# Kernel tuning notes

Measured on AMD Instinct MI355X. Metric: run time of the kernel, lower is better.

The kernel has to match this reference:

```python
import jax, jax.numpy as jnp
import numpy as np

N, IN_C, OUT_C = 4096, 256, 64
ALPHA = 0.2  # LeakyReLU negative slope


def setup_inputs() -> dict:
    key = jax.random.key(0)
    k1, k2, k3, k4 = jax.random.split(key, 4)
    H = jax.random.normal(k1, (N, IN_C), dtype=jnp.float32)
    adj = jax.random.randint(k2, (N, N), 0, 2, dtype=jnp.int32)
    # xavier_uniform with gain=1.414
    gain = 1.414
    limW = gain * np.sqrt(6.0 / (IN_C + OUT_C))
    W = jax.random.uniform(k3, (IN_C, OUT_C), minval=-limW, maxval=limW, dtype=jnp.float32)
    lima = gain * np.sqrt(6.0 / (2 * OUT_C + 1))
    a = jax.random.uniform(k4, (2 * OUT_C, 1), minval=-lima, maxval=lima, dtype=jnp.float32)
    return {"H": H, "adj": adj, "W": W, "a": a}


def reference(H, adj, W, a):
    Wh = H @ W  # [N, out_C]
    # Attention_Mat[i,j] = concat(Wh_i, Wh_j); score = Attention_Mat @ a
    # = (Wh @ a1)_i + (Wh @ a2)_j  -- fused, avoids the O(N^2 * 2F) tensor.
    a1, a2 = a[:OUT_C, 0], a[OUT_C:, 0]
    e = (Wh @ a1)[:, None] + (Wh @ a2)[None, :]  # [N, N]
    e = jnp.where(e > 0, e, ALPHA * e)  # LeakyReLU
    att = jax.nn.softmax(e, axis=1)
    # NOTE: original masks AFTER softmax (rows are not renormalized).
    att = jnp.where(adj > 0, att, jnp.zeros_like(att))
    out = att @ Wh  # [N, out_C]
    return jax.nn.elu(out)  # concat=True
```

## Files before the change

kernel.cpp:

```cpp
#include <hip/hip_runtime.h>
#include <math.h>

static constexpr int NN   = 4096;
static constexpr int INC  = 256;
static constexpr int OUTC = 64;

typedef _Float16 half8 __attribute__((ext_vector_type(8)));
typedef float floatx4 __attribute__((ext_vector_type(4)));

__device__ __forceinline__ float lrelu(float x) {
    return fmaxf(x, 0.f) + 0.2f * fminf(x, 0.f);
}
__device__ __forceinline__ float elu1(float x) {
    return x > 0.f ? x : (__expf(x) - 1.f);
}

__global__ __launch_bounds__(256) void k_prep(const int* __restrict__ adj,
                                              unsigned int* __restrict__ bits,
                                              const float* __restrict__ H,
                                              const float* __restrict__ W,
                                              const float* __restrict__ a,
                                              unsigned short* __restrict__ WhT,
                                              float* __restrict__ f1,
                                              float* __restrict__ f2) {
    const int t = threadIdx.x;
    if (blockIdx.x >= 256) {
        const int tau = (blockIdx.x - 256) * 256 + t;
        const int4* src = (const int4*)adj + (size_t)tau * 8;
        unsigned int o = 0;
        #pragma unroll
        for (int u = 0; u < 8; ++u) {
            const int4 v = src[u];
            const unsigned int nib = (unsigned int)(v.x > 0)
                                   | ((unsigned int)(v.y > 0) << 1)
                                   | ((unsigned int)(v.z > 0) << 2)
                                   | ((unsigned int)(v.w > 0) << 3);
            o |= nib << (4 * u);
        }
        bits[tau] = o;
        return;
    }
    __shared__ __align__(16) float Hl[16 * INC];
    __shared__ _Float16 Tl[16 * 68];
    const int i0 = blockIdx.x * 16;
    {
        const float4* H4 = (const float4*)(H + i0 * INC);
        float4* Hl4 = (float4*)Hl;
        #pragma unroll
        for (int u = 0; u < 4; ++u) Hl4[u * 256 + t] = H4[u * 256 + t];
    }
    __syncthreads();
    const int c = t & 63;
    const int g = t >> 6;
    const float a1c = a[c];
    const float a2c = a[OUTC + c];
    float acc[4] = {0.f, 0.f, 0.f, 0.f};
    const float4* Hl4 = (const float4*)Hl;
    #pragma unroll 4
    for (int k4 = 0; k4 < INC / 4; ++k4) {
        const float w0 = W[(k4 * 4 + 0) * OUTC + c];
        const float w1 = W[(k4 * 4 + 1) * OUTC + c];
        const float w2 = W[(k4 * 4 + 2) * OUTC + c];
        const float w3 = W[(k4 * 4 + 3) * OUTC + c];
        #pragma unroll
        for (int s = 0; s < 4; ++s) {
            const float4 h = Hl4[(g + 4 * s) * (INC / 4) + k4];
            acc[s] = fmaf(h.x, w0, fmaf(h.y, w1, fmaf(h.z, w2, fmaf(h.w, w3, acc[s]))));
        }
    }
    #pragma unroll
    for (int s = 0; s < 4; ++s) {
        const int r = g + 4 * s;
        Tl[r * 68 + c] = (_Float16)acc[s];
        float v1 = acc[s] * a1c;
        float v2 = acc[s] * a2c;
        #pragma unroll
        for (int off = 32; off; off >>= 1) {
            v1 += __shfl_xor(v1, off);
            v2 += __shfl_xor(v2, off);
        }
        if (c == 0) { f1[i0 + r] = v1; f2[i0 + r] = v2; }
    }
    __syncthreads();
    const int c2 = t >> 2;
    const int rs = (t & 3) * 4;
    ushort4 u;
    u.x = *(const unsigned short*)&Tl[(rs + 0) * 68 + c2];
    u.y = *(const unsigned short*)&Tl[(rs + 1) * 68 + c2];
    u.z = *(const unsigned short*)&Tl[(rs + 2) * 68 + c2];
    u.w = *(const unsigned short*)&Tl[(rs + 3) * 68 + c2];
    *(ushort4*)(WhT + c2 * NN + i0 + rs) = u;
}

__global__ __launch_bounds__(1024, 4) void k_att(const unsigned char* __restrict__ bits,
                                                 const _Float16* __restrict__ WhT,
                                                 const float* __restrict__ f1,
                                                 const float* __restrict__ f2,
                                                 float* __restrict__ out) {
    __shared__ __align__(16) float sf2[NN];
    __shared__ __align__(16) float sacc[16 * 1024];
    __shared__ float sden[16 * 16];
    __shared__ float smax[16];
    const int t = threadIdx.x;
    const int w = t >> 6;
    const int l = t & 63;
    const int m = l & 15;
    const int quad = l >> 4;
    const int i0 = blockIdx.x * 16;

    {
        const float4 v = ((const float4*)f2)[t];
        ((float4*)sf2)[t] = v;
        float mloc = fmaxf(fmaxf(v.x, v.y), fmaxf(v.z, v.w));
        #pragma unroll
        for (int off = 32; off; off >>= 1) mloc = fmaxf(mloc, __shfl_xor(mloc, off));
        if (l == 0) smax[w] = mloc;
    }
    __syncthreads();
    float maxf2 = smax[0];
    #pragma unroll
    for (int k = 1; k < 16; ++k) maxf2 = fmaxf(maxf2, smax[k]);

    const float f1r = f1[i0 + m];
    const float mrow = lrelu(f1r + maxf2);
    float den = 0.f;
    floatx4 acc[4] = {{0.f,0.f,0.f,0.f},{0.f,0.f,0.f,0.f},{0.f,0.f,0.f,0.f},{0.f,0.f,0.f,0.f}};
    const int jbase = w * 32 + quad * 8;
    const unsigned char* brow = bits + (size_t)(i0 + m) * (NN / 8) + (jbase >> 3);
    unsigned int m8[8];
    #pragma unroll
    for (int it = 0; it < 8; ++it) m8[it] = brow[it * 64];

    #pragma unroll 2
    for (int it = 0; it < 8; ++it) {
        const int j = jbase + it * 512;
        const unsigned int mb = m8[it];
        const float4 g0 = *(const float4*)(sf2 + j);
        const float4 g1 = *(const float4*)(sf2 + j + 4);
        half8 af;
        {
            float p;
            p = __expf(lrelu(f1r + g0.x) - mrow); den += p; af[0] = (mb & 1u)   ? (_Float16)p : (_Float16)0.f;
            p = __expf(lrelu(f1r + g0.y) - mrow); den += p; af[1] = (mb & 2u)   ? (_Float16)p : (_Float16)0.f;
            p = __expf(lrelu(f1r + g0.z) - mrow); den += p; af[2] = (mb & 4u)   ? (_Float16)p : (_Float16)0.f;
            p = __expf(lrelu(f1r + g0.w) - mrow); den += p; af[3] = (mb & 8u)   ? (_Float16)p : (_Float16)0.f;
            p = __expf(lrelu(f1r + g1.x) - mrow); den += p; af[4] = (mb & 16u)  ? (_Float16)p : (_Float16)0.f;
            p = __expf(lrelu(f1r + g1.y) - mrow); den += p; af[5] = (mb & 32u)  ? (_Float16)p : (_Float16)0.f;
            p = __expf(lrelu(f1r + g1.z) - mrow); den += p; af[6] = (mb & 64u)  ? (_Float16)p : (_Float16)0.f;
            p = __expf(lrelu(f1r + g1.w) - mrow); den += p; af[7] = (mb & 128u) ? (_Float16)p : (_Float16)0.f;
        }
        #pragma unroll
        for (int nt = 0; nt < 4; ++nt) {
            const half8 bf = *(const half8*)(WhT + (size_t)(nt * 16 + m) * NN + j);
            acc[nt] = __builtin_amdgcn_mfma_f32_16x16x32_f16(af, bf, acc[nt], 0, 0, 0);
        }
    }
    den += __shfl_xor(den, 16);
    den += __shfl_xor(den, 32);
    if (l < 16) sden[w * 16 + l] = den;
    #pragma unroll
    for (int nt = 0; nt < 4; ++nt)
        #pragma unroll
        for (int r = 0; r < 4; ++r)
            sacc[w * 1024 + (quad * 4 + r) * 64 + nt * 16 + m] = acc[nt][r];
    __syncthreads();
    float s = 0.f;
    #pragma unroll
    for (int w2 = 0; w2 < 16; ++w2) s += sacc[w2 * 1024 + t];
    float dden = 0.f;
    const int row = t >> 6;
    #pragma unroll
    for (int w2 = 0; w2 < 16; ++w2) dden += sden[w2 * 16 + row];
    out[(size_t)i0 * OUTC + t] = elu1(s / dden);
}

extern "C" void kernel_launch(void* const* d_in, const int* in_sizes, int n_in,
                              void* d_out, int out_size, void* d_ws, size_t ws_size,
                              hipStream_t stream) {
    const float* H  = (const float*)d_in[0];
    const int* adj  = (const int*)d_in[1];
    const float* W  = (const float*)d_in[2];
    const float* a  = (const float*)d_in[3];
    float* out = (float*)d_out;
    char* ws = (char*)d_ws;
    unsigned short* WhT = (unsigned short*)(ws);
    float* f1 = (float*)(ws + (512 << 10));
    float* f2 = (float*)(ws + (528 << 10));
    unsigned int* bits = (unsigned int*)(ws + (1 << 20));
    hipLaunchKernelGGL(k_prep, dim3(2304), dim3(256), 0, stream,
                       adj, bits, H, W, a, WhT, f1, f2);
    hipLaunchKernelGGL(k_att,  dim3(256),  dim3(1024), 0, stream,
                       (const unsigned char*)bits, (const _Float16*)WhT, f1, f2, out);
}
```

Measured before the change: 123.5 us.

## Fuse prep and attention kernels into one cooperative kernel with grid sync

Merges the projection/mask-packing kernel and the attention kernel into a single cooperative launch separated by a grid-wide barrier. Each block now packs the adjacency bits for its own 16 rows straight into shared memory, so the packed mask no longer makes a round trip through global memory. f1 also stays in shared memory. The cost is a grid synchronization, a less coalesced per-wave adjacency read pattern, and a Wh computation that reads W from global per thread instead of staging H in shared memory.

```diff
diff --git a/kernel.cpp b/kernel.cpp
--- a/kernel.cpp
+++ b/kernel.cpp
@@ -1,5 +1,8 @@
 #include <hip/hip_runtime.h>
+#include <hip/hip_cooperative_groups.h>
 #include <math.h>
+
+namespace cg = cooperative_groups;
 
 static constexpr int NN   = 4096;
 static constexpr int INC  = 256;
@@ -15,101 +18,84 @@
     return x > 0.f ? x : (__expf(x) - 1.f);
 }
 
-__global__ __launch_bounds__(256) void k_prep(const int* __restrict__ adj,
-                                              unsigned int* __restrict__ bits,
-                                              const float* __restrict__ H,
-                                              const float* __restrict__ W,
-                                              const float* __restrict__ a,
-                                              unsigned short* __restrict__ WhT,
-                                              float* __restrict__ f1,
-                                              float* __restrict__ f2) {
+__global__ __launch_bounds__(1024, 4) void k_gat(const int* __restrict__ adj,
+                                                 const float* __restrict__ H,
+                                                 const float* __restrict__ W,
+                                                 const float* __restrict__ a,
+                                                 unsigned short* __restrict__ WhT,
+                                                 float* __restrict__ f2g,
+                                                 float* __restrict__ out) {
+    __shared__ __align__(16) float sf2[NN];
+    __shared__ __align__(16) float sacc[16 * 1024];
+    __shared__ __align__(8) unsigned long long smask[16 * 65];
+    __shared__ float sden[16 * 16];
+    __shared__ float smax[16];
+    __shared__ float sf1[16];
+
     const int t = threadIdx.x;
-    if (blockIdx.x >= 256) {
-        const int tau = (blockIdx.x - 256) * 256 + t;
-        const int4* src = (const int4*)adj + (size_t)tau * 8;
-        unsigned int o = 0;
-        #pragma unroll
-        for (int u = 0; u < 8; ++u) {
-            const int4 v = src[u];
-            const unsigned int nib = (unsigned int)(v.x > 0)
-                                   | ((unsigned int)(v.y > 0) << 1)
-                                   | ((unsigned int)(v.z > 0) << 2)
-                                   | ((unsigned int)(v.w > 0) << 3);
-            o |= nib << (4 * u);
+    const int w = t >> 6;
+    const int l = t & 63;
+    const int i0 = blockIdx.x * 16;
+    const int row = i0 + w;
+
+    {
+        const int4* ap = (const int4*)(adj + (size_t)row * NN) + l * 16;
+        unsigned long long bits = 0ull;
+        #pragma unroll 4
+        for (int k = 0; k < 16; ++k) {
+            const int4 v = ap[k];
+            const unsigned long long nib =
+                  (unsigned long long)(v.x > 0)
+                | ((unsigned long long)(v.y > 0) << 1)
+                | ((unsigned long long)(v.z > 0) << 2)
+                | ((unsigned long long)(v.w > 0) << 3);
+            bits |= nib << (4 * k);
         }
-        bits[tau] = o;
-        return;
+        smask[w * 65 + l] = bits;
     }
-    __shared__ __align__(16) float Hl[16 * INC];
-    __shared__ _Float16 Tl[16 * 68];
-    const int i0 = blockIdx.x * 16;
+
     {
-        const float4* H4 = (const float4*)(H + i0 * INC);
-        float4* Hl4 = (float4*)Hl;
-        #pragma unroll
-        for (int u = 0; u < 4; ++u) Hl4[u * 256 + t] = H4[u * 256 + t];
-    }
-    __syncthreads();
-    const int c = t & 63;
-    const int g = t >> 6;
-    const float a1c = a[c];
-    const float a2c = a[OUTC + c];
-    float acc[4] = {0.f, 0.f, 0.f, 0.f};
-    const float4* Hl4 = (const float4*)Hl;
-    #pragma unroll 4
-    for (int k4 = 0; k4 < INC / 4; ++k4) {
-        const float w0 = W[(k4 * 4 + 0) * OUTC + c];
-        const float w1 = W[(k4 * 4 + 1) * OUTC + c];
-        const float w2 = W[(k4 * 4 + 2) * OUTC + c];
-        const float w3 = W[(k4 * 4 + 3) * OUTC + c];
-        #pragma unroll
-        for (int s = 0; s < 4; ++s) {
-            const float4 h = Hl4[(g + 4 * s) * (INC / 4) + k4];
-            acc[s] = fmaf(h.x, w0, fmaf(h.y, w1, fmaf(h.z, w2, fmaf(h.w, w3, acc[s]))));
+        _Float16* Tl = (_Float16*)sacc;
+        const int c = l;
+        const float4* Hr = (const float4*)(H + (size_t)row * INC);
+        float acc = 0.f;
+        #pragma unroll 8
+        for (int k4 = 0; k4 < INC / 4; ++k4) {
+            const float4 h = Hr[k4];
+            acc = fmaf(h.x, W[(k4 * 4 + 0) * OUTC + c],
+                  fmaf(h.y, W[(k4 * 4 + 1) * OUTC + c],
+                  fmaf(h.z, W[(k4 * 4 + 2) * OUTC + c],
+                  fmaf(h.w, W[(k4 * 4 + 3) * OUTC + c], acc))));
         }
-    }
-    #pragma unroll
-    for (int s = 0; s < 4; ++s) {
-        const int r = g + 4 * s;
-        Tl[r * 68 + c] = (_Float16)acc[s];
-        float v1 = acc[s] * a1c;
-        float v2 = acc[s] * a2c;
+        Tl[w * 68 + c] = (_Float16)acc;
+        float v1 = acc * a[c];
+        float v2 = acc * a[OUTC + c];
         #pragma unroll
         for (int off = 32; off; off >>= 1) {
             v1 += __shfl_xor(v1, off);
             v2 += __shfl_xor(v2, off);
         }
-        if (c == 0) { f1[i0 + r] = v1; f2[i0 + r] = v2; }
+        if (c == 0) { sf1[w] = v1; f2g[row] = v2; }
+        __syncthreads();
+        if (t < 256) {
+            const int c2 = t >> 2;
+            const int rs = (t & 3) * 4;
+            ushort4 u;
+            u.x = *(const unsigned short*)&Tl[(rs + 0) * 68 + c2];
+            u.y = *(const unsigned short*)&Tl[(rs + 1) * 68 + c2];
+            u.z = *(const unsigned short*)&Tl[(rs + 2) * 68 + c2];
+            u.w = *(const unsigned short*)&Tl[(rs + 3) * 68 + c2];
+            *(ushort4*)(WhT + (size_t)c2 * NN + i0 + rs) = u;
+        }
     }
-    __syncthreads();
-    const int c2 = t >> 2;
-    const int rs = (t & 3) * 4;
-    ushort4 u;
-    u.x = *(const unsigned short*)&Tl[(rs + 0) * 68 + c2];
-    u.y = *(const unsigned short*)&Tl[(rs + 1) * 68 + c2];
-    u.z = *(const unsigned short*)&Tl[(rs + 2) * 68 + c2];
-    u.w = *(const unsigned short*)&Tl[(rs + 3) * 68 + c2];
-    *(ushort4*)(WhT + c2 * NN + i0 + rs) = u;
-}
+    __threadfence();
+    cg::this_grid().sync();
 
-__global__ __launch_bounds__(1024, 4) void k_att(const unsigned char* __restrict__ bits,
-                                                 const _Float16* __restrict__ WhT,
-                                                 const float* __restrict__ f1,
-                                                 const float* __restrict__ f2,
-                                                 float* __restrict__ out) {
-    __shared__ __align__(16) float sf2[NN];
-    __shared__ __align__(16) float sacc[16 * 1024];
-    __shared__ float sden[16 * 16];
-    __shared__ float smax[16];
-    const int t = threadIdx.x;
-    const int w = t >> 6;
-    const int l = t & 63;
     const int m = l & 15;
     const int quad = l >> 4;
-    const int i0 = blockIdx.x * 16;
 
     {
-        const float4 v = ((const float4*)f2)[t];
+        const float4 v = ((const float4*)f2g)[t];
         ((float4*)sf2)[t] = v;
         float mloc = fmaxf(fmaxf(v.x, v.y), fmaxf(v.z, v.w));
         #pragma unroll
@@ -121,20 +107,17 @@
     #pragma unroll
     for (int k = 1; k < 16; ++k) maxf2 = fmaxf(maxf2, smax[k]);
 
-    const float f1r = f1[i0 + m];
+    const float f1r = sf1[m];
     const float mrow = lrelu(f1r + maxf2);
     float den = 0.f;
     floatx4 acc[4] = {{0.f,0.f,0.f,0.f},{0.f,0.f,0.f,0.f},{0.f,0.f,0.f,0.f},{0.f,0.f,0.f,0.f}};
     const int jbase = w * 32 + quad * 8;
-    const unsigned char* brow = bits + (size_t)(i0 + m) * (NN / 8) + (jbase >> 3);
-    unsigned int m8[8];
-    #pragma unroll
-    for (int it = 0; it < 8; ++it) m8[it] = brow[it * 64];
+    const unsigned char* mrow_p = (const unsigned char*)smask + m * 520 + w * 4 + quad;
 
     #pragma unroll 2
     for (int it = 0; it < 8; ++it) {
         const int j = jbase + it * 512;
-        const unsigned int mb = m8[it];
+        const unsigned int mb = mrow_p[it * 64];
         const float4 g0 = *(const float4*)(sf2 + j);
         const float4 g1 = *(const float4*)(sf2 + j + 4);
         half8 af;
@@ -168,9 +151,9 @@
     #pragma unroll
     for (int w2 = 0; w2 < 16; ++w2) s += sacc[w2 * 1024 + t];
     float dden = 0.f;
-    const int row = t >> 6;
+    const int orow = t >> 6;
     #pragma unroll
-    for (int w2 = 0; w2 < 16; ++w2) dden += sden[w2 * 16 + row];
+    for (int w2 = 0; w2 < 16; ++w2) dden += sden[w2 * 16 + orow];
     out[(size_t)i0 * OUTC + t] = elu1(s / dden);
 }
 
@@ -184,11 +167,9 @@
     float* out = (float*)d_out;
     char* ws = (char*)d_ws;
     unsigned short* WhT = (unsigned short*)(ws);
-    float* f1 = (float*)(ws + (512 << 10));
-    float* f2 = (float*)(ws + (528 << 10));
-    unsigned int* bits = (unsigned int*)(ws + (1 << 20));
-    hipLaunchKernelGGL(k_prep, dim3(2304), dim3(256), 0, stream,
-                       adj, bits, H, W, a, WhT, f1, f2);
-    hipLaunchKernelGGL(k_att,  dim3(256),  dim3(1024), 0, stream,
-                       (const unsigned char*)bits, (const _Float16*)WhT, f1, f2, out);
+    float* f2g = (float*)(ws + (512 << 10));
+
+    void* args[] = { (void*)&adj, (void*)&H, (void*)&W, (void*)&a,
+                     (void*)&WhT, (void*)&f2g, (void*)&out };
+    hipLaunchCooperativeKernel((void*)k_gat, dim3(256), dim3(1024), args, 0, stream);
 }
```

Result: slower. 248.9 us (+101.5%).

## Fuse adjacency bitmask packing into attention kernel with double-buffered ballot masks

Applied to the files above, without the earlier changes.

Drops the separate adjacency-to-bitmask pass and its bits workspace. The attention kernel now reads the int adjacency rows directly, packs them into 64-bit masks with wave ballots into a double-buffered shared array, and prefetches the next 512-column chunk while the current chunk's MFMAs run. This removes writing and re-reading the packed bitmask and one kernel's worth of grid work, at the cost of a block-wide barrier every iteration and adjacency traffic now inside the compute kernel, limited to 256 blocks.

```diff
diff --git a/kernel.cpp b/kernel.cpp
--- a/kernel.cpp
+++ b/kernel.cpp
@@ -15,33 +15,15 @@
     return x > 0.f ? x : (__expf(x) - 1.f);
 }
 
-__global__ __launch_bounds__(256) void k_prep(const int* __restrict__ adj,
-                                              unsigned int* __restrict__ bits,
-                                              const float* __restrict__ H,
-                                              const float* __restrict__ W,
-                                              const float* __restrict__ a,
-                                              unsigned short* __restrict__ WhT,
-                                              float* __restrict__ f1,
-                                              float* __restrict__ f2) {
-    const int t = threadIdx.x;
-    if (blockIdx.x >= 256) {
-        const int tau = (blockIdx.x - 256) * 256 + t;
-        const int4* src = (const int4*)adj + (size_t)tau * 8;
-        unsigned int o = 0;
-        #pragma unroll
-        for (int u = 0; u < 8; ++u) {
-            const int4 v = src[u];
-            const unsigned int nib = (unsigned int)(v.x > 0)
-                                   | ((unsigned int)(v.y > 0) << 1)
-                                   | ((unsigned int)(v.z > 0) << 2)
-                                   | ((unsigned int)(v.w > 0) << 3);
-            o |= nib << (4 * u);
-        }
-        bits[tau] = o;
-        return;
-    }
+__global__ __launch_bounds__(256) void k_wh(const float* __restrict__ H,
+                                            const float* __restrict__ W,
+                                            const float* __restrict__ a,
+                                            unsigned short* __restrict__ WhT,
+                                            float* __restrict__ f1,
+                                            float* __restrict__ f2) {
     __shared__ __align__(16) float Hl[16 * INC];
     __shared__ _Float16 Tl[16 * 68];
+    const int t = threadIdx.x;
     const int i0 = blockIdx.x * 16;
     {
         const float4* H4 = (const float4*)(H + i0 * INC);
@@ -92,13 +74,14 @@
     *(ushort4*)(WhT + c2 * NN + i0 + rs) = u;
 }
 
-__global__ __launch_bounds__(1024, 4) void k_att(const unsigned char* __restrict__ bits,
+__global__ __launch_bounds__(1024, 4) void k_att(const int* __restrict__ adj,
                                                  const _Float16* __restrict__ WhT,
                                                  const float* __restrict__ f1,
                                                  const float* __restrict__ f2,
                                                  float* __restrict__ out) {
     __shared__ __align__(16) float sf2[NN];
     __shared__ __align__(16) float sacc[16 * 1024];
+    __shared__ __align__(8) unsigned long long smask[2][16][9];
     __shared__ float sden[16 * 16];
     __shared__ float smax[16];
     const int t = threadIdx.x;
@@ -116,25 +99,37 @@
         for (int off = 32; off; off >>= 1) mloc = fmaxf(mloc, __shfl_xor(mloc, off));
         if (l == 0) smax[w] = mloc;
     }
+
+    const int* arow = adj + (size_t)(i0 + w) * NN;
+    int pv[8];
+    #pragma unroll
+    for (int e = 0; e < 8; ++e) pv[e] = arow[e * 64 + l];
+    #pragma unroll
+    for (int e = 0; e < 8; ++e) {
+        const unsigned long long bm = __ballot(pv[e] > 0);
+        if (l == 0) smask[0][w][e] = bm;
+    }
     __syncthreads();
+
     float maxf2 = smax[0];
     #pragma unroll
     for (int k = 1; k < 16; ++k) maxf2 = fmaxf(maxf2, smax[k]);
-
     const float f1r = f1[i0 + m];
     const float mrow = lrelu(f1r + maxf2);
+
     float den = 0.f;
     floatx4 acc[4] = {{0.f,0.f,0.f,0.f},{0.f,0.f,0.f,0.f},{0.f,0.f,0.f,0.f},{0.f,0.f,0.f,0.f}};
-    const int jbase = w * 32 + quad * 8;
-    const unsigned char* brow = bits + (size_t)(i0 + m) * (NN / 8) + (jbase >> 3);
-    unsigned int m8[8];
-    #pragma unroll
-    for (int it = 0; it < 8; ++it) m8[it] = brow[it * 64];
+    const int jb = w * 32 + quad * 8;
+    const unsigned char* mbase = (const unsigned char*)&smask[0][0][0]
+                               + m * 72 + (w >> 1) * 8 + (w & 1) * 4 + quad;
 
-    #pragma unroll 2
-    for (int it = 0; it < 8; ++it) {
-        const int j = jbase + it * 512;
-        const unsigned int mb = m8[it];
+    for (int tt = 0; tt < 8; ++tt) {
+        if (tt < 7) {
+            #pragma unroll
+            for (int e = 0; e < 8; ++e) pv[e] = arow[(tt + 1) * 512 + e * 64 + l];
+        }
+        const int j = tt * 512 + jb;
+        const unsigned int mb = mbase[(tt & 1) * (16 * 72)];
         const float4 g0 = *(const float4*)(sf2 + j);
         const float4 g1 = *(const float4*)(sf2 + j + 4);
         half8 af;
@@ -154,7 +149,16 @@
             const half8 bf = *(const half8*)(WhT + (size_t)(nt * 16 + m) * NN + j);
             acc[nt] = __builtin_amdgcn_mfma_f32_16x16x32_f16(af, bf, acc[nt], 0, 0, 0);
         }
+        if (tt < 7) {
+            #pragma unroll
+            for (int e = 0; e < 8; ++e) {
+                const unsigned long long bm = __ballot(pv[e] > 0);
+                if (l == 0) smask[(tt + 1) & 1][w][e] = bm;
+            }
+        }
+        __syncthreads();
     }
+
     den += __shfl_xor(den, 16);
     den += __shfl_xor(den, 32);
     if (l < 16) sden[w * 16 + l] = den;
@@ -168,9 +172,9 @@
     #pragma unroll
     for (int w2 = 0; w2 < 16; ++w2) s += sacc[w2 * 1024 + t];
     float dden = 0.f;
-    const int row = t >> 6;
+    const int orow = t >> 6;
     #pragma unroll
-    for (int w2 = 0; w2 < 16; ++w2) dden += sden[w2 * 16 + row];
+    for (int w2 = 0; w2 < 16; ++w2) dden += sden[w2 * 16 + orow];
     out[(size_t)i0 * OUTC + t] = elu1(s / dden);
 }
 
@@ -186,9 +190,7 @@
     unsigned short* WhT = (unsigned short*)(ws);
     float* f1 = (float*)(ws + (512 << 10));
     float* f2 = (float*)(ws + (528 << 10));
-    unsigned int* bits = (unsigned int*)(ws + (1 << 20));
-    hipLaunchKernelGGL(k_prep, dim3(2304), dim3(256), 0, stream,
-                       adj, bits, H, W, a, WhT, f1, f2);
-    hipLaunchKernelGGL(k_att,  dim3(256),  dim3(1024), 0, stream,
-                       (const unsigned char*)bits, (const _Float16*)WhT, f1, f2, out);
+    hipLaunchKernelGGL(k_wh,  dim3(256), dim3(256),  0, stream, H, W, a, WhT, f1, f2);
+    hipLaunchKernelGGL(k_att, dim3(256), dim3(1024), 0, stream,
+                       adj, (const _Float16*)WhT, f1, f2, out);
 }
```

Result: slower. 127.5 us (+3.2%).
